# Kernel tuning notes

Hardware: AMD Instinct MI355X
Metric: run time of the kernel (lower is better)

The kernel has to match this reference:

```python
import jax, jax.numpy as jnp
import numpy as np

WS = (4, 4, 4)          # window size per axis
DISP = (2, 2, 2)        # cyclic-shift displacement = window_size // 2
HEADS = 8
HEAD_DIM = 32
DIM = 256


def _make_mask(x_shift, y_shift, z_shift):
    wx, wy, wz = WS
    dx, dy, dz = DISP
    m = np.zeros((wx, wy, wz, wx, wy, wz), np.float32)
    if x_shift:
        m[-dx:, :, :, :-dx, :, :] = -np.inf
        m[:-dx, :, :, -dx:, :, :] = -np.inf
    if y_shift:
        m[:, -dy:, :, :, :-dy, :] = -np.inf
        m[:, :-dy, :, :, -dy:, :] = -np.inf
    if z_shift:
        m[:, :, -dz:, :, :, :-dz] = -np.inf
        m[:, :, :-dz, :, :, -dz:] = -np.inf
    W = wx * wy * wz
    return jnp.asarray(m.reshape(W, W))


def setup_inputs() -> dict:
    key = jax.random.key(0)
    k1, k2, k3 = jax.random.split(key, 3)
    inner = HEADS * HEAD_DIM
    x = jax.random.normal(k1, (1, 48, 48, 48, DIM), jnp.float32)
    w_qkv = jax.random.normal(k2, (DIM, 3 * inner), jnp.float32) * (DIM ** -0.5)
    w_out = jax.random.normal(k3, (inner, DIM), jnp.float32) * (inner ** -0.5)
    b_out = jnp.zeros((DIM,), jnp.float32)
    return {"x": x, "w_qkv": w_qkv, "w_out": w_out, "b_out": b_out}


def reference(x, w_qkv, w_out, b_out):
    wx, wy, wz = WS
    h, d = HEADS, HEAD_DIM
    scale = d ** -0.5
    xm = _make_mask(True, False, False)
    ym = _make_mask(False, True, False)
    zm = _make_mask(False, False, True)

    # cyclic shift
    x = jnp.roll(x, (-DISP[0], -DISP[1], -DISP[2]), axis=(1, 2, 3))
    b, nx, ny, nz, _ = x.shape
    nwx, nwy, nwz = nx // wx, ny // wy, nz // wz
    W = wx * wy * wz
    nw = nwx * nwy * nwz

    qkv = x @ w_qkv                      # [b,nx,ny,nz,3*h*d]
    q, k, v = jnp.split(qkv, 3, axis=-1)

    def win(t):
        t = t.reshape(b, nwx, wx, nwy, wy, nwz, wz, h, d)
        t = t.transpose(0, 7, 1, 3, 5, 2, 4, 6, 8)   # b h nwx nwy nwz wx wy wz d
        return t.reshape(b, h, nw, W, d)

    q, k, v = win(q), win(k), win(v)
    dots = jnp.einsum('bhwid,bhwjd->bhwij', q, k) * scale

    # additive shift masks on the last window along each axis
    dots = dots.reshape(b, h, nwx, nwy, nwz, W, W)
    dots = dots.at[:, :, -1, :, :].add(xm)
    dots = dots.at[:, :, :, -1, :].add(ym)
    dots = dots.at[:, :, :, :, -1].add(zm)
    # faithful replication of original einops label mismatch: the tensor is
    # (nwx,nwy,nwz) but is flattened as if labeled (n_y,n_z,n_x) -> (n_x n_y n_z),
    # i.e. actual flatten order (nwz, nwx, nwy)
    dots = dots.transpose(0, 1, 4, 2, 3, 5, 6).reshape(b, h, nw, W, W)

    attn = jax.nn.softmax(dots, axis=-1)
    out = jnp.einsum('bhwij,bhwjd->bhwid', attn, v)

    out = out.reshape(b, h, nwx, nwy, nwz, wx, wy, wz, d)
    out = out.transpose(0, 2, 5, 3, 6, 4, 7, 1, 8).reshape(b, nx, ny, nz, h * d)
    out = out @ w_out + b_out
    # cyclic back shift
    return jnp.roll(out, DISP, axis=(1, 2, 3))
```

## Files before the change

### kernel.cpp

```cpp
#include <hip/hip_runtime.h>
#include <hip/hip_bf16.h>

typedef __attribute__((ext_vector_type(8))) short short8;
typedef __attribute__((ext_vector_type(4))) float f32x4;

#define NT 110592

static __device__ __forceinline__ unsigned int f2bf(float f){
  unsigned int x; __builtin_memcpy(&x,&f,4);
  x += 0x7fffu + ((x>>16)&1u);
  return x >> 16;
}

static __device__ __forceinline__ void gll16(const unsigned short* g, unsigned short* l){
  typedef const __attribute__((address_space(1))) unsigned int gu32;
  typedef __attribute__((address_space(3))) unsigned int lu32;
  __builtin_amdgcn_global_load_lds((gu32*)(const void*)g, (lu32*)(void*)l, 16, 0, 0);
}

__global__ void xconv(const float* __restrict__ x, unsigned short* __restrict__ o){
  size_t i = ((size_t)blockIdx.x*256 + threadIdx.x) * 8;
  float4 a = *(const float4*)(x+i), b = *(const float4*)(x+i+4);
  uint4 pk;
  pk.x = f2bf(a.x)|(f2bf(a.y)<<16); pk.y = f2bf(a.z)|(f2bf(a.w)<<16);
  pk.z = f2bf(b.x)|(f2bf(b.y)<<16); pk.w = f2bf(b.z)|(f2bf(b.w)<<16);
  *(uint4*)(o+i) = pk;
}

__global__ void tpose(const float* __restrict__ in, unsigned short* __restrict__ out,
                      int R, int Cc){
  int id = blockIdx.x*256 + threadIdx.x;
  if (id < R*Cc){ int r = id / Cc, c = id - r*Cc; out[c*R + r] = (unsigned short)f2bf(in[id]); }
}

template<bool CF32>
__global__ __launch_bounds__(256) void gemm_bt(
    const unsigned short* __restrict__ A,
    const unsigned short* __restrict__ Bt,
    const float* __restrict__ bias,
    void* __restrict__ Cv,
    int M, int N, int K)
{
  __shared__ __align__(16) unsigned short As[2*128*32];
  __shared__ __align__(16) unsigned short Bs[2*128*32];

  const int nwg = gridDim.x;
  const int bid = blockIdx.x;
  const int qq = nwg >> 3, rr = nwg & 7;
  const int xcd = bid & 7, loc = bid >> 3;
  const int swz = (xcd < rr ? xcd*(qq+1) : rr*(qq+1) + (xcd-rr)*qq) + loc;
  const int nbn = N >> 7;
  const int bn = swz % nbn;
  const int bm = swz / nbn;

  const int tid  = threadIdx.x;
  const int lane = tid & 63;
  const int wave = tid >> 6;
  const int wm = wave >> 1, wn = wave & 1;
  const int l16 = lane & 15, q = lane >> 4;

  const size_t arow0 = (size_t)(bm*128 + (tid>>2))*K;
  const size_t brow0 = (size_t)(bn*128 + (tid>>2))*K;
  const int g8  = ((tid&3) ^ ((tid>>3)&3)) * 8;
  const int cg8 = (q ^ ((l16>>1)&3)) * 8;

  f32x4 acc[4][4] = {};

  for (int k0 = 0; k0 < K; k0 += 64){
    __syncthreads();
    gll16(A  + arow0 + k0 + g8,                      &As[tid*8]);
    gll16(A  + arow0 + (size_t)64*K + k0 + g8,       &As[(tid+256)*8]);
    gll16(A  + arow0 + k0 + 32 + g8,                 &As[4096 + tid*8]);
    gll16(A  + arow0 + (size_t)64*K + k0 + 32 + g8,  &As[4096 + (tid+256)*8]);
    gll16(Bt + brow0 + k0 + g8,                      &Bs[tid*8]);
    gll16(Bt + brow0 + (size_t)64*K + k0 + g8,       &Bs[(tid+256)*8]);
    gll16(Bt + brow0 + k0 + 32 + g8,                 &Bs[4096 + tid*8]);
    gll16(Bt + brow0 + (size_t)64*K + k0 + 32 + g8,  &Bs[4096 + (tid+256)*8]);
    __syncthreads();

    #pragma unroll
    for (int h = 0; h < 2; ++h){
      short8 af[4], bfm[4];
      #pragma unroll
      for (int t = 0; t < 4; ++t){
        af[t]  = *(const short8*)&As[h*4096 + (wm*64 + t*16 + l16)*32 + cg8];
        bfm[t] = *(const short8*)&Bs[h*4096 + (wn*64 + t*16 + l16)*32 + cg8];
      }
      #pragma unroll
      for (int im = 0; im < 4; ++im)
        #pragma unroll
        for (int in = 0; in < 4; ++in)
          acc[im][in] = __builtin_amdgcn_mfma_f32_16x16x32_bf16(af[im], bfm[in], acc[im][in], 0, 0, 0);
    }
  }

  #pragma unroll
  for (int in = 0; in < 4; ++in){
    int col = bn*128 + wn*64 + in*16 + l16;
    float bv = CF32 ? bias[col] : 0.f;
    #pragma unroll
    for (int im = 0; im < 4; ++im){
      int row0 = bm*128 + wm*64 + im*16 + q*4;
      #pragma unroll
      for (int r = 0; r < 4; ++r){
        if (CF32) ((float*)Cv)[(size_t)(row0 + r)*N + col] = acc[im][in][r] + bv;
        else ((unsigned short*)Cv)[(size_t)(row0 + r)*N + col] = (unsigned short)f2bf(acc[im][in][r]);
      }
    }
  }
}

__global__ __launch_bounds__(256) void attn3d(
    const unsigned short* __restrict__ qkv,
    unsigned short* __restrict__ aout)
{
  __shared__ __align__(16) unsigned short sh[4*6912];
  const int tid  = threadIdx.x;
  const int wave = tid >> 6, lane = tid & 63;
  const int l16  = lane & 15, q = lane >> 4;
  unsigned short* P  = sh + wave*6912;
  unsigned short* VT = P + 64*72;

  const int wh   = blockIdx.x*4 + wave;
  const int head = wh & 7;
  const int w    = wh >> 3;
  const int A  = w / 144;
  const int B  = (w / 12) % 12;
  const int Cw = w % 12;

  const int iyy = l16 >> 2, izz = l16 & 3;
  int tok_qk[4], tok_v[4];
  #pragma unroll
  for (int t = 0; t < 4; ++t){
    int px = (4*B  + t   + 2) % 48;
    int py = (4*Cw + iyy + 2) % 48;
    int pz = (4*A  + izz + 2) % 48;
    tok_qk[t] = (px*48 + py)*48 + pz;
    int vx = (4*A  + t   + 2) % 48;
    int vy = (4*B  + iyy + 2) % 48;
    int vz = (4*Cw + izz + 2) % 48;
    tok_v[t] = (vx*48 + vy)*48 + vz;
  }

  {
    int sx = (4*A  + (lane>>4)     + 2) % 48;
    int sy = (4*B  + ((lane>>2)&3) + 2) % 48;
    int sz = (4*Cw + (lane&3)      + 2) % 48;
    const unsigned short* vp = qkv + (size_t)((sx*48+sy)*48+sz)*768 + 512 + head*32;
    uint4 v0 = *(const uint4*)(vp);
    uint4 v1 = *(const uint4*)(vp+8);
    uint4 v2 = *(const uint4*)(vp+16);
    uint4 v3 = *(const uint4*)(vp+24);
    unsigned vv[16] = {v0.x,v0.y,v0.z,v0.w, v1.x,v1.y,v1.z,v1.w,
                       v2.x,v2.y,v2.z,v2.w, v3.x,v3.y,v3.z,v3.w};
    #pragma unroll
    for (int u = 0; u < 16; ++u){
      VT[(2*u+0)*72 + lane] = (unsigned short)(vv[u] & 0xffffu);
      VT[(2*u+1)*72 + lane] = (unsigned short)(vv[u] >> 16);
    }
  }

  short8 kf[4], qf[4];
  #pragma unroll
  for (int t = 0; t < 4; ++t){
    const unsigned short* base = qkv + (size_t)tok_qk[t]*768 + head*32 + q*8;
    qf[t] = *(const short8*)(base);
    kf[t] = *(const short8*)(base + 256);
  }

  f32x4 s[4][4] = {};
  #pragma unroll
  for (int im = 0; im < 4; ++im)
    #pragma unroll
    for (int jn = 0; jn < 4; ++jn)
      s[im][jn] = __builtin_amdgcn_mfma_f32_16x16x32_bf16(kf[im], qf[jn], s[im][jn], 0, 0, 0);

  const float scale = 0.17677669529663687f;
  const int mx = (B == 11), my = (Cw == 11), mz = (A == 11);
  const int dy = my & ((q>>1) ^ (l16>>3));
  float sum4[4] = {0.f,0.f,0.f,0.f};
  #pragma unroll
  for (int jn = 0; jn < 4; ++jn){
    #pragma unroll
    for (int im = 0; im < 4; ++im){
      const int dxy = (mx & ((im>>1) ^ (jn>>1))) | dy;
      float e0 = (dxy | (mz & (0 ^ ((l16>>1)&1)))) ? 0.f : __expf(s[im][jn][0]*scale);
      float e1 = (dxy | (mz & (0 ^ ((l16>>1)&1)))) ? 0.f : __expf(s[im][jn][1]*scale);
      float e2 = (dxy | (mz & (1 ^ ((l16>>1)&1)))) ? 0.f : __expf(s[im][jn][2]*scale);
      float e3 = (dxy | (mz & (1 ^ ((l16>>1)&1)))) ? 0.f : __expf(s[im][jn][3]*scale);
      sum4[jn] += (e0+e1)+(e2+e3);
      uint2 pk;
      pk.x = f2bf(e0) | (f2bf(e1)<<16);
      pk.y = f2bf(e2) | (f2bf(e3)<<16);
      *(uint2*)&P[(jn*16+l16)*72 + im*16 + q*4] = pk;
    }
  }
  #pragma unroll
  for (int jn = 0; jn < 4; ++jn){
    float sj = sum4[jn];
    sj += __shfl_xor(sj, 16);
    sj += __shfl_xor(sj, 32);
    sum4[jn] = 1.f / sj;
  }

  f32x4 o[2][4] = {};
  #pragma unroll
  for (int ks = 0; ks < 2; ++ks){
    short8 vf[2], pf[4];
    #pragma unroll
    for (int dt = 0; dt < 2; ++dt)
      vf[dt] = *(const short8*)&VT[(dt*16 + l16)*72 + ks*32 + q*8];
    #pragma unroll
    for (int it = 0; it < 4; ++it)
      pf[it] = *(const short8*)&P[(it*16 + l16)*72 + ks*32 + q*8];
    #pragma unroll
    for (int dt = 0; dt < 2; ++dt)
      #pragma unroll
      for (int it = 0; it < 4; ++it)
        o[dt][it] = __builtin_amdgcn_mfma_f32_16x16x32_bf16(vf[dt], pf[it], o[dt][it], 0, 0, 0);
  }

  #pragma unroll
  for (int it = 0; it < 4; ++it){
    float inv = sum4[it];
    unsigned short* op = aout + (size_t)tok_v[it]*256 + head*32;
    #pragma unroll
    for (int dt = 0; dt < 2; ++dt){
      uint2 pk;
      pk.x = f2bf(o[dt][it][0]*inv) | (f2bf(o[dt][it][1]*inv) << 16);
      pk.y = f2bf(o[dt][it][2]*inv) | (f2bf(o[dt][it][3]*inv) << 16);
      *(uint2*)(op + dt*16 + q*4) = pk;
    }
  }
}

extern "C" void kernel_launch(void* const* d_in, const int* in_sizes, int n_in,
                              void* d_out, int out_size, void* d_ws, size_t ws_size,
                              hipStream_t stream) {
  const float* x     = (const float*)d_in[0];
  const float* w_qkv = (const float*)d_in[1];
  const float* w_out = (const float*)d_in[2];
  const float* b_out = (const float*)d_in[3];
  float* out = (float*)d_out;

  unsigned short* qkv   = (unsigned short*)d_ws;
  unsigned short* xbf   = qkv   + (size_t)NT*768;
  unsigned short* aout  = xbf;
  unsigned short* wqkvT = xbf   + (size_t)NT*256;
  unsigned short* woutT = wqkvT + (size_t)768*256;

  xconv<<<dim3(NT*256/2048), dim3(256), 0, stream>>>(x, xbf);
  tpose<<<dim3((256*768 + 255)/256), dim3(256), 0, stream>>>(w_qkv, wqkvT, 256, 768);
  tpose<<<dim3((256*256 + 255)/256), dim3(256), 0, stream>>>(w_out, woutT, 256, 256);

  gemm_bt<false><<<dim3((768/128)*(NT/128)), dim3(256), 0, stream>>>(xbf, wqkvT, nullptr, qkv, NT, 768, 256);

  attn3d<<<dim3(13824/4), dim3(256), 0, stream>>>(qkv, aout);

  gemm_bt<true><<<dim3((256/128)*(NT/128)), dim3(256), 0, stream>>>(aout, woutT, b_out, out, NT, 256, 256);
}
```

Before: 360.9 us.

## Keep full B tile resident in LDS and stream A strips from registers

Replaces the K-looped double-tile GEMM with a kernel that loads the whole 128x256 weight slice into LDS once per block. Each block then processes two 128-row strips of A, with each wave loading its A fragments straight from global memory into registers, so there are no per-K-step barriers. This removes repeated B staging and the synchronisation inside the loop. In exchange it uses 64KB of LDS per block, which limits occupancy, and A is read without LDS sharing or coalescing across lanes.

```diff
diff --git a/kernel.cpp b/kernel.cpp
--- a/kernel.cpp
+++ b/kernel.cpp
@@ -34,15 +34,14 @@
 }
 
 template<bool CF32>
-__global__ __launch_bounds__(256) void gemm_bt(
+__global__ __launch_bounds__(256) void gemm_bres(
     const unsigned short* __restrict__ A,
     const unsigned short* __restrict__ Bt,
     const float* __restrict__ bias,
     void* __restrict__ Cv,
-    int M, int N, int K)
+    int M, int N, int SPB)
 {
-  __shared__ __align__(16) unsigned short As[2*128*32];
-  __shared__ __align__(16) unsigned short Bs[2*128*32];
+  __shared__ __align__(16) unsigned short Bs[128*256];
 
   const int nwg = gridDim.x;
   const int bid = blockIdx.x;
@@ -51,60 +50,67 @@
   const int swz = (xcd < rr ? xcd*(qq+1) : rr*(qq+1) + (xcd-rr)*qq) + loc;
   const int nbn = N >> 7;
   const int bn = swz % nbn;
-  const int bm = swz / nbn;
+  const int mc = swz / nbn;
 
   const int tid  = threadIdx.x;
   const int lane = tid & 63;
   const int wave = tid >> 6;
-  const int wm = wave >> 1, wn = wave & 1;
   const int l16 = lane & 15, q = lane >> 4;
-
-  const size_t arow0 = (size_t)(bm*128 + (tid>>2))*K;
-  const size_t brow0 = (size_t)(bn*128 + (tid>>2))*K;
-  const int g8  = ((tid&3) ^ ((tid>>3)&3)) * 8;
-  const int cg8 = (q ^ ((l16>>1)&3)) * 8;
-
-  f32x4 acc[4][4] = {};
-
-  for (int k0 = 0; k0 < K; k0 += 64){
-    __syncthreads();
-    gll16(A  + arow0 + k0 + g8,                      &As[tid*8]);
-    gll16(A  + arow0 + (size_t)64*K + k0 + g8,       &As[(tid+256)*8]);
-    gll16(A  + arow0 + k0 + 32 + g8,                 &As[4096 + tid*8]);
-    gll16(A  + arow0 + (size_t)64*K + k0 + 32 + g8,  &As[4096 + (tid+256)*8]);
-    gll16(Bt + brow0 + k0 + g8,                      &Bs[tid*8]);
-    gll16(Bt + brow0 + (size_t)64*K + k0 + g8,       &Bs[(tid+256)*8]);
-    gll16(Bt + brow0 + k0 + 32 + g8,                 &Bs[4096 + tid*8]);
-    gll16(Bt + brow0 + (size_t)64*K + k0 + 32 + g8,  &Bs[4096 + (tid+256)*8]);
-    __syncthreads();
-
-    #pragma unroll
-    for (int h = 0; h < 2; ++h){
-      short8 af[4], bfm[4];
-      #pragma unroll
-      for (int t = 0; t < 4; ++t){
-        af[t]  = *(const short8*)&As[h*4096 + (wm*64 + t*16 + l16)*32 + cg8];
-        bfm[t] = *(const short8*)&Bs[h*4096 + (wn*64 + t*16 + l16)*32 + cg8];
-      }
-      #pragma unroll
-      for (int im = 0; im < 4; ++im)
+  const int cg  = ((q ^ ((l16>>1)&3)) << 3);
+
+  #pragma unroll
+  for (int rnd = 0; rnd < 16; ++rnd){
+    int u   = rnd*256 + tid;
+    int row = u >> 5;
+    int w   = u & 31;
+    int kf  = w >> 2, g = w & 3;
+    int col = kf*32 + ((g ^ ((row>>1)&3)) << 3);
+    gll16(Bt + (size_t)(bn*128 + row)*256 + col, &Bs[(size_t)u*8]);
+  }
+  __syncthreads();
+
+  float bv[8];
+  if (CF32){
+    #pragma unroll
+    for (int tn = 0; tn < 8; ++tn) bv[tn] = bias[bn*128 + tn*16 + l16];
+  }
+
+  for (int t = 0; t < SPB; ++t){
+    const int strip = mc*SPB + t;
+    const unsigned short* Ab = A + (size_t)(strip*128 + wave*32)*256;
+
+    short8 af[2][8];
+    #pragma unroll
+    for (int tm = 0; tm < 2; ++tm)
+      #pragma unroll
+      for (int kf = 0; kf < 8; ++kf)
+        af[tm][kf] = *(const short8*)(Ab + (size_t)(tm*16 + l16)*256 + kf*32 + q*8);
+
+    f32x4 acc[2][8] = {};
+    #pragma unroll
+    for (int kf = 0; kf < 8; ++kf){
+      short8 bfm[8];
+      #pragma unroll
+      for (int tn = 0; tn < 8; ++tn)
+        bfm[tn] = *(const short8*)&Bs[(tn*16 + l16)*256 + kf*32 + cg];
+      #pragma unroll
+      for (int tm = 0; tm < 2; ++tm)
         #pragma unroll
-        for (int in = 0; in < 4; ++in)
-          acc[im][in] = __builtin_amdgcn_mfma_f32_16x16x32_bf16(af[im], bfm[in], acc[im][in], 0, 0, 0);
-    }
-  }
-
-  #pragma unroll
-  for (int in = 0; in < 4; ++in){
-    int col = bn*128 + wn*64 + in*16 + l16;
-    float bv = CF32 ? bias[col] : 0.f;
-    #pragma unroll
-    for (int im = 0; im < 4; ++im){
-      int row0 = bm*128 + wm*64 + im*16 + q*4;
-      #pragma unroll
-      for (int r = 0; r < 4; ++r){
-        if (CF32) ((float*)Cv)[(size_t)(row0 + r)*N + col] = acc[im][in][r] + bv;
-        else ((unsigned short*)Cv)[(size_t)(row0 + r)*N + col] = (unsigned short)f2bf(acc[im][in][r]);
+        for (int tn = 0; tn < 8; ++tn)
+          acc[tm][tn] = __builtin_amdgcn_mfma_f32_16x16x32_bf16(af[tm][kf], bfm[tn], acc[tm][tn], 0, 0, 0);
+    }
+
+    #pragma unroll
+    for (int tn = 0; tn < 8; ++tn){
+      int col = bn*128 + tn*16 + l16;
+      #pragma unroll
+      for (int tm = 0; tm < 2; ++tm){
+        int row0 = strip*128 + wave*32 + tm*16 + q*4;
+        #pragma unroll
+        for (int r = 0; r < 4; ++r){
+          if (CF32) ((float*)Cv)[(size_t)(row0 + r)*N + col] = acc[tm][tn][r] + bv[tn];
+          else ((unsigned short*)Cv)[(size_t)(row0 + r)*N + col] = (unsigned short)f2bf(acc[tm][tn][r]);
+        }
       }
     }
   }
@@ -253,9 +259,9 @@
   tpose<<<dim3((256*768 + 255)/256), dim3(256), 0, stream>>>(w_qkv, wqkvT, 256, 768);
   tpose<<<dim3((256*256 + 255)/256), dim3(256), 0, stream>>>(w_out, woutT, 256, 256);
 
-  gemm_bt<false><<<dim3((768/128)*(NT/128)), dim3(256), 0, stream>>>(xbf, wqkvT, nullptr, qkv, NT, 768, 256);
+  gemm_bres<false><<<dim3(432*6), dim3(256), 0, stream>>>(xbf, wqkvT, nullptr, qkv, NT, 768, 2);
 
   attn3d<<<dim3(13824/4), dim3(256), 0, stream>>>(qkv, aout);
 
-  gemm_bt<true><<<dim3((256/128)*(NT/128)), dim3(256), 0, stream>>>(aout, woutT, b_out, out, NT, 256, 256);
-}
+  gemm_bres<true><<<dim3(432*2), dim3(256), 0, stream>>>(aout, woutT, b_out, out, NT, 256, 2);
+}
```

Measured after the change: 417.5 us. 15.7% more time.

## Double-buffer LDS tiles in bf16 GEMM to overlap loads with MFMA

Applied to the files above, without the earlier changes.

Doubles the LDS buffers for the A and B tiles and prefetches the next K-slab with global_load_lds while MFMAs run on the current one. This removes one of the two barriers per iteration and is meant to hide global-load latency behind compute. LDS use doubles to 64KB per block, which may cut occupancy. The only remaining barrier sits after the compute, and no explicit vmcnt wait is visible, so the async loads must already be complete at that barrier for correctness.

```diff
diff --git a/kernel.cpp b/kernel.cpp
--- a/kernel.cpp
+++ b/kernel.cpp
@@ -41,8 +41,8 @@
     void* __restrict__ Cv,
     int M, int N, int K)
 {
-  __shared__ __align__(16) unsigned short As[2*128*32];
-  __shared__ __align__(16) unsigned short Bs[2*128*32];
+  __shared__ __align__(16) unsigned short As[2*8192];
+  __shared__ __align__(16) unsigned short Bs[2*8192];
 
   const int nwg = gridDim.x;
   const int bid = blockIdx.x;
@@ -66,25 +66,33 @@
 
   f32x4 acc[4][4] = {};
 
+  auto stage = [&](int k0, int cur){
+    unsigned short* Ad = &As[cur*8192];
+    unsigned short* Bd = &Bs[cur*8192];
+    gll16(A  + arow0 + k0 + g8,                      &Ad[tid*8]);
+    gll16(A  + arow0 + (size_t)64*K + k0 + g8,       &Ad[(tid+256)*8]);
+    gll16(A  + arow0 + k0 + 32 + g8,                 &Ad[4096 + tid*8]);
+    gll16(A  + arow0 + (size_t)64*K + k0 + 32 + g8,  &Ad[4096 + (tid+256)*8]);
+    gll16(Bt + brow0 + k0 + g8,                      &Bd[tid*8]);
+    gll16(Bt + brow0 + (size_t)64*K + k0 + g8,       &Bd[(tid+256)*8]);
+    gll16(Bt + brow0 + k0 + 32 + g8,                 &Bd[4096 + (tid)*8]);
+    gll16(Bt + brow0 + (size_t)64*K + k0 + 32 + g8,  &Bd[4096 + (tid+256)*8]);
+  };
+
+  stage(0, 0);
+  __syncthreads();
+
+  int cur = 0;
   for (int k0 = 0; k0 < K; k0 += 64){
-    __syncthreads();
-    gll16(A  + arow0 + k0 + g8,                      &As[tid*8]);
-    gll16(A  + arow0 + (size_t)64*K + k0 + g8,       &As[(tid+256)*8]);
-    gll16(A  + arow0 + k0 + 32 + g8,                 &As[4096 + tid*8]);
-    gll16(A  + arow0 + (size_t)64*K + k0 + 32 + g8,  &As[4096 + (tid+256)*8]);
-    gll16(Bt + brow0 + k0 + g8,                      &Bs[tid*8]);
-    gll16(Bt + brow0 + (size_t)64*K + k0 + g8,       &Bs[(tid+256)*8]);
-    gll16(Bt + brow0 + k0 + 32 + g8,                 &Bs[4096 + tid*8]);
-    gll16(Bt + brow0 + (size_t)64*K + k0 + 32 + g8,  &Bs[4096 + (tid+256)*8]);
-    __syncthreads();
+    if (k0 + 64 < K) stage(k0 + 64, cur ^ 1);
 
     #pragma unroll
     for (int h = 0; h < 2; ++h){
       short8 af[4], bfm[4];
       #pragma unroll
       for (int t = 0; t < 4; ++t){
-        af[t]  = *(const short8*)&As[h*4096 + (wm*64 + t*16 + l16)*32 + cg8];
-        bfm[t] = *(const short8*)&Bs[h*4096 + (wn*64 + t*16 + l16)*32 + cg8];
+        af[t]  = *(const short8*)&As[cur*8192 + h*4096 + (wm*64 + t*16 + l16)*32 + cg8];
+        bfm[t] = *(const short8*)&Bs[cur*8192 + h*4096 + (wn*64 + t*16 + l16)*32 + cg8];
       }
       #pragma unroll
       for (int im = 0; im < 4; ++im)
@@ -92,6 +100,9 @@
         for (int in = 0; in < 4; ++in)
           acc[im][in] = __builtin_amdgcn_mfma_f32_16x16x32_bf16(af[im], bfm[in], acc[im][in], 0, 0, 0);
     }
+
+    if (k0 + 64 < K) __syncthreads();
+    cur ^= 1;
   }
 
   #pragma unroll
```

Result: slower. 368.1 us (+2.0%).
